# Optimization experiments

Hardware: AMD Instinct MI355X
Metric: run time of the kernel (lower is better)

Reference implementation:

```python
import jax, jax.numpy as jnp
import numpy as np

N_NODES = 20000
N_EDGES = 320000
N_GRAPHS = 64
OBS = 64
EDGE_DIM = 16
HEADS = 4
HID = 64
NEG_SLOPE = 0.2
EPS = 1e-16


def _gat_layer(x, src, dst, edge_attr, W, We, att_src, att_dst, att_edge, b):
    """PyG GATConv (concat=True, eval mode: no dropout).
    x: [N, Fin], edge_attr: [E, De], W: [Fin, H*C], We: [De, H*C],
    att_*: [H, C], b: [H*C]. Returns [N, H*C]."""
    N = x.shape[0]
    h = (x @ W).reshape(N, HEADS, HID)                      # [N,H,C]
    he = (edge_attr @ We).reshape(-1, HEADS, HID)           # [E,H,C]
    a_src = jnp.einsum('nhc,hc->nh', h, att_src)            # [N,H]
    a_dst = jnp.einsum('nhc,hc->nh', h, att_dst)
    a_e = jnp.einsum('ehc,hc->eh', he, att_edge)            # [E,H]
    alpha = a_src[src] + a_dst[dst] + a_e                   # [E,H]
    alpha = jax.nn.leaky_relu(alpha, NEG_SLOPE)
    # segment softmax over destination neighborhoods
    m = jax.ops.segment_max(alpha, dst, num_segments=N)     # [N,H]
    m = jnp.where(jnp.isfinite(m), m, 0.0)
    ea = jnp.exp(alpha - m[dst])
    denom = jax.ops.segment_sum(ea, dst, num_segments=N)    # [N,H]
    alpha = ea / (denom[dst] + EPS)
    msg = h[src] * alpha[:, :, None]                        # [E,H,C]
    out = jax.ops.segment_sum(msg, dst, num_segments=N)     # [N,H,C]
    return out.reshape(N, HEADS * HID) + b


def _make_params(key):
    ks = jax.random.split(key, 18)
    p = {}
    dims_in = [OBS, HEADS * HID, HEADS * HID]
    for i in range(3):
        j = i * 6
        fin = dims_in[i]
        p[f'W{i+1}'] = jax.random.normal(ks[j], (fin, HEADS * HID), jnp.float32) * (1.0 / np.sqrt(fin))
        p[f'We{i+1}'] = jax.random.normal(ks[j+1], (EDGE_DIM, HEADS * HID), jnp.float32) * (1.0 / np.sqrt(EDGE_DIM))
        p[f'att_src{i+1}'] = jax.random.normal(ks[j+2], (HEADS, HID), jnp.float32) * 0.1
        p[f'att_dst{i+1}'] = jax.random.normal(ks[j+3], (HEADS, HID), jnp.float32) * 0.1
        p[f'att_edge{i+1}'] = jax.random.normal(ks[j+4], (HEADS, HID), jnp.float32) * 0.1
        p[f'b{i+1}'] = jnp.zeros((HEADS * HID,), jnp.float32)
    return p


def setup_inputs() -> dict:
    key = jax.random.key(0)
    k1, k2, k3, k4, kp = jax.random.split(key, 5)
    inp = {
        'x': jax.random.normal(k1, (N_NODES, OBS), jnp.float32),
        'edge_index': jax.random.randint(k2, (2, N_EDGES), 0, N_NODES, jnp.int64),
        'edge_attr': jax.random.normal(k3, (N_EDGES, EDGE_DIM), jnp.float32),
        'batch': jnp.sort(jax.random.randint(k4, (N_NODES,), 0, N_GRAPHS, jnp.int64)),
    }
    inp.update(_make_params(kp))
    return inp


def reference(x, edge_index, edge_attr, batch,
              W1, We1, att_src1, att_dst1, att_edge1, b1,
              W2, We2, att_src2, att_dst2, att_edge2, b2,
              W3, We3, att_src3, att_dst3, att_edge3, b3):
    src, dst = edge_index[0], edge_index[1]
    h = jax.nn.relu(_gat_layer(x, src, dst, edge_attr, W1, We1, att_src1, att_dst1, att_edge1, b1))
    h = jax.nn.relu(_gat_layer(h, src, dst, edge_attr, W2, We2, att_src2, att_dst2, att_edge2, b2))
    h = jax.nn.relu(_gat_layer(h, src, dst, edge_attr, W3, We3, att_src3, att_dst3, att_edge3, b3))
    # global mean pool over graphs
    sums = jax.ops.segment_sum(h, batch, num_segments=N_GRAPHS)      # [G, H*C]
    counts = jax.ops.segment_sum(jnp.ones((h.shape[0], 1), h.dtype), batch, num_segments=N_GRAPHS)
    pooled = sums / jnp.maximum(counts, 1.0)
    return jnp.tanh(pooled)
```

## Files before the change

### kernel.cpp

```cpp
#include <hip/hip_runtime.h>
#include <hip/hip_bf16.h>
#include <hip/hip_fp16.h>
#include <math.h>

#define N_NODES 20000
#define N_EDGES 320000
#define N_GRAPHS 64
#define OBS 64
#define EDGE_DIM 16
#define HEADS 4
#define HID 64
#define HC 256
#define NEG_SLOPE 0.2f
#define EPSF 1e-16f
#define N_SCAN_BLOCKS ((N_NODES + 255) / 256)
#define CVT_BLOCKS (N_NODES * OBS / 4 / 256)
#define CAP 64

typedef _Float16 f16x8 __attribute__((ext_vector_type(8)));
typedef float f32x4 __attribute__((ext_vector_type(4)));

__global__ __launch_bounds__(256) void zero3_kernel(int* __restrict__ counts,
                                                    float* __restrict__ pooled,
                                                    int* __restrict__ gcounts) {
    int i = blockIdx.x * 256 + threadIdx.x;
    if (i < N_NODES) counts[i] = 0;
    if (i < N_GRAPHS * HC) pooled[i] = 0.f;
    if (i < N_GRAPHS) gcounts[i] = 0;
}

__global__ __launch_bounds__(256) void cvtwt_kernel(const float* __restrict__ x, __half* __restrict__ x16,
                                                    const float* __restrict__ W0, const float* __restrict__ W1,
                                                    const float* __restrict__ W2,
                                                    __half* __restrict__ wt0, __half* __restrict__ wt1,
                                                    __half* __restrict__ wt2) {
    int b = blockIdx.x, t = threadIdx.x;
    if (b < CVT_BLOCKS) {
        int i = (b * 256 + t) * 4;
        float4 v = *(const float4*)(x + i);
        *(__half2*)(x16 + i)     = __floats2half2_rn(v.x, v.y);
        *(__half2*)(x16 + i + 2) = __floats2half2_rn(v.z, v.w);
    } else if (b < CVT_BLOCKS + OBS) {
        int k = b - CVT_BLOCKS;
        wt0[(size_t)t * OBS + k] = __float2half(W0[(size_t)k * HC + t]);
    } else if (b < CVT_BLOCKS + OBS + HC) {
        int k = b - CVT_BLOCKS - OBS;
        wt1[(size_t)t * HC + k] = __float2half(W1[(size_t)k * HC + t]);
    } else {
        int k = b - CVT_BLOCKS - OBS - HC;
        wt2[(size_t)t * HC + k] = __float2half(W2[(size_t)k * HC + t]);
    }
}

__global__ __launch_bounds__(256) void count_kernel(const int* __restrict__ ei, int* __restrict__ counts) {
    int e = blockIdx.x * 256 + threadIdx.x;
    if (e >= N_EDGES) return;
    atomicAdd(&counts[ei[N_EDGES + e]], 1);
}

__global__ __launch_bounds__(256) void scan_local_kernel(const int* __restrict__ counts,
                                                         int* __restrict__ row_start,
                                                         int* __restrict__ blk_tot) {
    int b = blockIdx.x, t = threadIdx.x;
    int i = b * 256 + t;
    int v = (i < N_NODES) ? counts[i] : 0;
    int lane = t & 63, w = t >> 6;
    int x = v;
    #pragma unroll
    for (int off = 1; off < 64; off <<= 1) {
        int y = __shfl_up(x, off, 64);
        if (lane >= off) x += y;
    }
    __shared__ int wsum[4];
    __shared__ int woff[4];
    if (lane == 63) wsum[w] = x;
    __syncthreads();
    if (t == 0) {
        int s = 0;
        #pragma unroll
        for (int k = 0; k < 4; ++k) { woff[k] = s; s += wsum[k]; }
        blk_tot[b] = s;
    }
    __syncthreads();
    if (i < N_NODES) row_start[i] = x - v + woff[w];
}

__global__ __launch_bounds__(256) void scan_add_kernel(int* __restrict__ row_start,
                                                       const int* __restrict__ blk_tot,
                                                       int* __restrict__ cursor) {
    __shared__ int sd[128];
    int b = blockIdx.x, t = threadIdx.x;
    if (t < 128) sd[t] = (t < b && t < N_SCAN_BLOCKS) ? blk_tot[t] : 0;
    __syncthreads();
    #pragma unroll
    for (int off = 64; off >= 1; off >>= 1) {
        if (t < off) sd[t] += sd[t + off];
        __syncthreads();
    }
    int base = sd[0];
    int i = b * 256 + t;
    if (i < N_NODES) {
        int r = row_start[i] + base;
        row_start[i] = r;
        cursor[i] = r;
    }
}

__global__ __launch_bounds__(256) void fill_kernel(const int* __restrict__ ei,
                                                   int* __restrict__ cursor,
                                                   int* __restrict__ src_csr,
                                                   int* __restrict__ edge_pos) {
    int e = blockIdx.x * 256 + threadIdx.x;
    if (e >= N_EDGES) return;
    int s = ei[e];
    int d = ei[N_EDGES + e];
    int pos = atomicAdd(&cursor[d], 1);
    src_csr[pos] = s;
    edge_pos[e] = pos;
}

__global__ void weff3_kernel(const float* __restrict__ We0, const float* __restrict__ ae0,
                             const float* __restrict__ We1, const float* __restrict__ ae1,
                             const float* __restrict__ We2, const float* __restrict__ ae2,
                             float* __restrict__ w_eff3) {
    int l = blockIdx.x, t = threadIdx.x;
    const float* We = (l == 0) ? We0 : (l == 1) ? We1 : We2;
    const float* ae = (l == 0) ? ae0 : (l == 1) ? ae1 : ae2;
    int hh = t >> 4, d = t & 15;
    float acc = 0.f;
    #pragma unroll 8
    for (int c = 0; c < HID; ++c)
        acc += We[d * HC + hh * HID + c] * ae[hh * HID + c];
    w_eff3[l * 64 + hh * 16 + d] = acc;
}

__global__ __launch_bounds__(256) void ae3_kernel(const float* __restrict__ edge_attr,
                                                  const int* __restrict__ edge_pos,
                                                  const float* __restrict__ w_eff3,
                                                  float4* __restrict__ ae_csr) {
    __shared__ float wsh[192];
    int t = threadIdx.x;
    if (t < 192) wsh[t] = w_eff3[t];
    __syncthreads();
    int e = blockIdx.x * 256 + t;
    if (e >= N_EDGES) return;
    const float* ea = edge_attr + (size_t)e * EDGE_DIM;
    float x[16];
    #pragma unroll
    for (int i = 0; i < 16; i += 4) {
        float4 v = *(const float4*)(ea + i);
        x[i] = v.x; x[i + 1] = v.y; x[i + 2] = v.z; x[i + 3] = v.w;
    }
    int pos = edge_pos[e];
    #pragma unroll
    for (int l = 0; l < 3; ++l) {
        float al[4];
        #pragma unroll
        for (int hh = 0; hh < 4; ++hh) {
            float acc = 0.f;
            #pragma unroll
            for (int i = 0; i < 16; ++i) acc += x[i] * wsh[l * 64 + hh * 16 + i];
            al[hh] = acc;
        }
        ae_csr[(size_t)l * N_EDGES + pos] = make_float4(al[0], al[1], al[2], al[3]);
    }
}

template <int NKT>
__global__ __launch_bounds__(256) void gemm16_kernel(const __half* __restrict__ A16,
                                                     const __half* __restrict__ Wt16,
                                                     __half* __restrict__ C16, int M,
                                                     const float* __restrict__ att_src,
                                                     const float* __restrict__ att_dst,
                                                     float* __restrict__ a_src,
                                                     float* __restrict__ a_dst) {
    constexpr int K = NKT * 32;
    __shared__ __align__(16) _Float16 lds[64 * 264];
    int t = threadIdx.x;
    int w = t >> 6, l = t & 63;
    int cg = l & 15, gg = l >> 4;
    int m0 = blockIdx.x * 64;

    {
        int row = (t >> 6) * 16 + (t & 15);
        int k8 = (t >> 4) & 3;
        int rg = m0 + row;
        if (rg >= M) rg = M - 1;
        const _Float16* ag = (const _Float16*)A16 + (size_t)rg * K + k8 * 8;
        f16x8 tmp[NKT];
        #pragma unroll
        for (int j = 0; j < NKT; ++j) tmp[j] = *(const f16x8*)(ag + j * 32);
        #pragma unroll
        for (int j = 0; j < NKT; ++j) *(f16x8*)&lds[(size_t)(j * 256 + t) * 8] = tmp[j];
    }
    __syncthreads();

    f32x4 acc[4][4] = {};
    const _Float16* bg = (const _Float16*)Wt16 + (size_t)(w * 64 + cg) * K + gg * 8;
    #pragma unroll 2
    for (int kt = 0; kt < NKT; ++kt) {
        f16x8 bf[4], af[4];
        #pragma unroll
        for (int ni = 0; ni < 4; ++ni)
            bf[ni] = *(const f16x8*)(bg + (size_t)(ni * 16) * K + kt * 32);
        #pragma unroll
        for (int mi = 0; mi < 4; ++mi)
            af[mi] = *(const f16x8*)&lds[(size_t)(kt * 256 + mi * 64 + l) * 8];
        #pragma unroll
        for (int mi = 0; mi < 4; ++mi)
            #pragma unroll
            for (int ni = 0; ni < 4; ++ni)
                acc[mi][ni] = __builtin_amdgcn_mfma_f32_16x16x32_f16(af[mi], bf[ni], acc[mi][ni], 0, 0, 0);
    }

    {
        float avs[4], avd[4];
        #pragma unroll
        for (int ni = 0; ni < 4; ++ni) {
            avs[ni] = att_src[w * 64 + ni * 16 + cg];
            avd[ni] = att_dst[w * 64 + ni * 16 + cg];
        }
        #pragma unroll
        for (int mi = 0; mi < 4; ++mi)
            #pragma unroll
            for (int reg = 0; reg < 4; ++reg) {
                float ps = acc[mi][0][reg] * avs[0] + acc[mi][1][reg] * avs[1]
                         + acc[mi][2][reg] * avs[2] + acc[mi][3][reg] * avs[3];
                float pd = acc[mi][0][reg] * avd[0] + acc[mi][1][reg] * avd[1]
                         + acc[mi][2][reg] * avd[2] + acc[mi][3][reg] * avd[3];
                #pragma unroll
                for (int o = 1; o < 16; o <<= 1) {
                    ps += __shfl_xor(ps, o, 64);
                    pd += __shfl_xor(pd, o, 64);
                }
                int m = m0 + mi * 16 + gg * 4 + reg;
                if (cg == 0 && m < M) {
                    a_src[(size_t)m * 4 + w] = ps;
                    a_dst[(size_t)m * 4 + w] = pd;
                }
            }
    }

    __syncthreads();
    #pragma unroll
    for (int mi = 0; mi < 4; ++mi)
        #pragma unroll
        for (int ni = 0; ni < 4; ++ni)
            #pragma unroll
            for (int reg = 0; reg < 4; ++reg) {
                int row = mi * 16 + gg * 4 + reg;
                int col = w * 64 + ni * 16 + cg;
                lds[row * 264 + col] = (_Float16)acc[mi][ni][reg];
            }
    __syncthreads();
    #pragma unroll
    for (int i = 0; i < 8; ++i) {
        int g = i * 256 + t;
        int row = g >> 5, cw = g & 31;
        int m = m0 + row;
        if (m < M) {
            f16x8 v = *(const f16x8*)&lds[row * 264 + cw * 8];
            *(f16x8*)((_Float16*)C16 + (size_t)m * HC + cw * 8) = v;
        }
    }
}

__global__ __launch_bounds__(256) void aggregate3_kernel(const int* __restrict__ src_csr,
                                                         const float4* __restrict__ ae_csr,
                                                         const int* __restrict__ row_start,
                                                         const int* __restrict__ counts,
                                                         const float* __restrict__ a_src,
                                                         const float* __restrict__ a_dst,
                                                         const __half* __restrict__ h16,
                                                         const float* __restrict__ bias,
                                                         __half* __restrict__ out16) {
    __shared__ float wlds[4][4][CAP + 1];
    int wid = threadIdx.x >> 6, lane = threadIdx.x & 63;
    int n = blockIdx.x * 4 + wid;
    int start = row_start[n];
    int deg = counts[n];
    const float4* ae = ae_csr + start;
    const int* sp = src_csr + start;
    float4 ad = *(const float4*)(a_dst + (size_t)n * 4);

    float m0 = -INFINITY, m1 = -INFINITY, m2 = -INFINITY, m3 = -INFINITY;
    for (int i = lane; i < deg; i += 64) {
        float4 a = ae[i];
        int s = sp[i];
        float4 as = *(const float4*)(a_src + (size_t)s * 4);
        float v0 = a.x + as.x + ad.x; v0 = v0 > 0.f ? v0 : NEG_SLOPE * v0;
        float v1 = a.y + as.y + ad.y; v1 = v1 > 0.f ? v1 : NEG_SLOPE * v1;
        float v2 = a.z + as.z + ad.z; v2 = v2 > 0.f ? v2 : NEG_SLOPE * v2;
        float v3 = a.w + as.w + ad.w; v3 = v3 > 0.f ? v3 : NEG_SLOPE * v3;
        if (i < CAP) {
            wlds[wid][0][i] = v0; wlds[wid][1][i] = v1;
            wlds[wid][2][i] = v2; wlds[wid][3][i] = v3;
        }
        m0 = fmaxf(m0, v0); m1 = fmaxf(m1, v1);
        m2 = fmaxf(m2, v2); m3 = fmaxf(m3, v3);
    }
    #pragma unroll
    for (int o = 32; o > 0; o >>= 1) {
        m0 = fmaxf(m0, __shfl_xor(m0, o, 64));
        m1 = fmaxf(m1, __shfl_xor(m1, o, 64));
        m2 = fmaxf(m2, __shfl_xor(m2, o, 64));
        m3 = fmaxf(m3, __shfl_xor(m3, o, 64));
    }

    float d0 = 0.f, d1 = 0.f, d2 = 0.f, d3 = 0.f;
    for (int i = lane; i < deg; i += 64) {
        float v0, v1, v2, v3;
        if (i < CAP) {
            v0 = wlds[wid][0][i]; v1 = wlds[wid][1][i];
            v2 = wlds[wid][2][i]; v3 = wlds[wid][3][i];
        } else {
            float4 a = ae[i];
            int s = sp[i];
            float4 as = *(const float4*)(a_src + (size_t)s * 4);
            v0 = a.x + as.x + ad.x; v0 = v0 > 0.f ? v0 : NEG_SLOPE * v0;
            v1 = a.y + as.y + ad.y; v1 = v1 > 0.f ? v1 : NEG_SLOPE * v1;
            v2 = a.z + as.z + ad.z; v2 = v2 > 0.f ? v2 : NEG_SLOPE * v2;
            v3 = a.w + as.w + ad.w; v3 = v3 > 0.f ? v3 : NEG_SLOPE * v3;
        }
        float e0 = __expf(v0 - m0);
        float e1 = __expf(v1 - m1);
        float e2 = __expf(v2 - m2);
        float e3 = __expf(v3 - m3);
        d0 += e0; d1 += e1; d2 += e2; d3 += e3;
        if (i < CAP) {
            wlds[wid][0][i] = e0; wlds[wid][1][i] = e1;
            wlds[wid][2][i] = e2; wlds[wid][3][i] = e3;
        }
    }
    #pragma unroll
    for (int o = 32; o > 0; o >>= 1) {
        d0 += __shfl_xor(d0, o, 64);
        d1 += __shfl_xor(d1, o, 64);
        d2 += __shfl_xor(d2, o, 64);
        d3 += __shfl_xor(d3, o, 64);
    }

    int g = lane >> 5, j = lane & 31;
    int head = j >> 3;
    float mh = (head < 2) ? (head == 0 ? m0 : m1) : (head == 2 ? m2 : m3);
    float dh = (head < 2) ? (head == 0 ? d0 : d1) : (head == 2 ? d2 : d3);
    float adh = (head < 2) ? (head == 0 ? ad.x : ad.y) : (head == 2 ? ad.z : ad.w);

    float acc[8] = {};
    int niter = (deg + 1) >> 1;
    #pragma unroll 2
    for (int it = 0; it < niter; ++it) {
        int e = it * 2 + g;
        bool valid = e < deg;
        int ec = valid ? e : deg - 1;
        int s = sp[ec];
        float wgt;
        if (ec < CAP) {
            wgt = wlds[wid][head][ec];
        } else {
            float4 a = ae[ec];
            float aa = (head < 2) ? (head == 0 ? a.x : a.y) : (head == 2 ? a.z : a.w);
            const float* asp = a_src + (size_t)s * 4;
            float v = aa + asp[head] + adh;
            v = v > 0.f ? v : NEG_SLOPE * v;
            wgt = __expf(v - mh);
        }
        if (!valid) wgt = 0.f;
        f16x8 hv = *(const f16x8*)((const _Float16*)h16 + (size_t)s * HC + j * 8);
        #pragma unroll
        for (int q = 0; q < 8; ++q) acc[q] += wgt * (float)hv[q];
    }
    #pragma unroll
    for (int q = 0; q < 8; ++q) acc[q] += __shfl_xor(acc[q], 32, 64);

    if (g == 0) {
        float invd = 1.f / (dh + EPSF);
        float4 b0 = *(const float4*)(bias + j * 8);
        float4 b1 = *(const float4*)(bias + j * 8 + 4);
        float r[8];
        r[0] = fmaxf(acc[0] * invd + b0.x, 0.f);
        r[1] = fmaxf(acc[1] * invd + b0.y, 0.f);
        r[2] = fmaxf(acc[2] * invd + b0.z, 0.f);
        r[3] = fmaxf(acc[3] * invd + b0.w, 0.f);
        r[4] = fmaxf(acc[4] * invd + b1.x, 0.f);
        r[5] = fmaxf(acc[5] * invd + b1.y, 0.f);
        r[6] = fmaxf(acc[6] * invd + b1.z, 0.f);
        r[7] = fmaxf(acc[7] * invd + b1.w, 0.f);
        f16x8 o;
        #pragma unroll
        for (int q = 0; q < 8; ++q) o[q] = (_Float16)r[q];
        *(f16x8*)((_Float16*)out16 + (size_t)n * HC + j * 8) = o;
    }
}

#define NPB 100
__global__ __launch_bounds__(256) void pool_kernel(const __half* __restrict__ h,
                                                   const int* __restrict__ batch,
                                                   float* __restrict__ pooled,
                                                   int* __restrict__ gcounts) {
    int t = threadIdx.x;
    int n0 = blockIdx.x * NPB;
    int n1 = n0 + NPB;
    if (n1 > N_NODES) n1 = N_NODES;
    if (n0 >= N_NODES) return;
    int cur = batch[n0];
    float acc = 0.f;
    int cnt = 0;
    for (int n = n0; n < n1; ++n) {
        int g = batch[n];
        if (g != cur) {
            atomicAdd(&pooled[cur * HC + t], acc);
            if (t == 0) atomicAdd(&gcounts[cur], cnt);
            acc = 0.f; cnt = 0; cur = g;
        }
        acc += __half2float(h[(size_t)n * HC + t]);
        cnt++;
    }
    atomicAdd(&pooled[cur * HC + t], acc);
    if (t == 0) atomicAdd(&gcounts[cur], cnt);
}

__global__ __launch_bounds__(256) void finalize_kernel(const float* __restrict__ pooled,
                                                       const int* __restrict__ gcounts,
                                                       float* __restrict__ out) {
    int g = blockIdx.x, t = threadIdx.x;
    float c = (float)(gcounts[g] > 1 ? gcounts[g] : 1);
    out[g * HC + t] = tanhf(pooled[g * HC + t] / c);
}

extern "C" void kernel_launch(void* const* d_in, const int* in_sizes, int n_in,
                              void* d_out, int out_size, void* d_ws, size_t ws_size,
                              hipStream_t stream) {
    const float* x         = (const float*)d_in[0];
    const int*   ei        = (const int*)d_in[1];
    const float* edge_attr = (const float*)d_in[2];
    const int*   batch     = (const int*)d_in[3];
    const float* Wl[3]  = {(const float*)d_in[4],  (const float*)d_in[10], (const float*)d_in[16]};
    const float* Wel[3] = {(const float*)d_in[5],  (const float*)d_in[11], (const float*)d_in[17]};
    const float* asl[3] = {(const float*)d_in[6],  (const float*)d_in[12], (const float*)d_in[18]};
    const float* adl[3] = {(const float*)d_in[7],  (const float*)d_in[13], (const float*)d_in[19]};
    const float* ael[3] = {(const float*)d_in[8],  (const float*)d_in[14], (const float*)d_in[20]};
    const float* bl[3]  = {(const float*)d_in[9],  (const float*)d_in[15], (const float*)d_in[21]};
    float* out = (float*)d_out;

    char* p = (char*)d_ws;
    auto alloc = [&](size_t bytes) -> void* {
        void* r = (void*)p;
        p += (bytes + 255) & ~(size_t)255;
        return r;
    };
    __half* x16       = (__half*)alloc((size_t)N_NODES * OBS * 2);
    __half* hA16      = (__half*)alloc((size_t)N_NODES * HC * 2);
    __half* hB16      = (__half*)alloc((size_t)N_NODES * HC * 2);
    __half* wt0       = (__half*)alloc((size_t)HC * OBS * 2);
    __half* wt1       = (__half*)alloc((size_t)HC * HC * 2);
    __half* wt2       = (__half*)alloc((size_t)HC * HC * 2);
    float* a_src      = (float*)alloc((size_t)N_NODES * 4 * 4);
    float* a_dst      = (float*)alloc((size_t)N_NODES * 4 * 4);
    float4* ae_csr    = (float4*)alloc((size_t)3 * N_EDGES * 16);
    int* counts       = (int*)alloc((size_t)N_NODES * 4);
    int* row_start    = (int*)alloc((size_t)N_NODES * 4);
    int* cursor       = (int*)alloc((size_t)N_NODES * 4);
    int* src_csr      = (int*)alloc((size_t)N_EDGES * 4);
    int* edge_pos     = (int*)alloc((size_t)N_EDGES * 4);
    float* w_eff3     = (float*)alloc(192 * 4);
    float* pooled     = (float*)alloc((size_t)N_GRAPHS * HC * 4);
    int* gcounts      = (int*)alloc((size_t)N_GRAPHS * 4);
    int* blk_tot      = (int*)alloc((size_t)N_SCAN_BLOCKS * 4);

    zero3_kernel<<<N_SCAN_BLOCKS, 256, 0, stream>>>(counts, pooled, gcounts);
    cvtwt_kernel<<<CVT_BLOCKS + OBS + HC + HC, 256, 0, stream>>>(x, x16, Wl[0], Wl[1], Wl[2],
                                                                 wt0, wt1, wt2);
    weff3_kernel<<<3, 64, 0, stream>>>(Wel[0], ael[0], Wel[1], ael[1], Wel[2], ael[2], w_eff3);

    count_kernel<<<N_EDGES / 256, 256, 0, stream>>>(ei, counts);
    scan_local_kernel<<<N_SCAN_BLOCKS, 256, 0, stream>>>(counts, row_start, blk_tot);
    scan_add_kernel<<<N_SCAN_BLOCKS, 256, 0, stream>>>(row_start, blk_tot, cursor);
    fill_kernel<<<N_EDGES / 256, 256, 0, stream>>>(ei, cursor, src_csr, edge_pos);

    ae3_kernel<<<N_EDGES / 256, 256, 0, stream>>>(edge_attr, edge_pos, w_eff3, ae_csr);

    const int ngrid = (N_NODES + 63) / 64;
    const __half* wtl[3] = {wt0, wt1, wt2};
    const __half* cur_in = x16;
    for (int l = 0; l < 3; ++l) {
        if (l == 0)
            gemm16_kernel<2><<<ngrid, 256, 0, stream>>>(cur_in, wtl[l], hA16, N_NODES,
                                                        asl[l], adl[l], a_src, a_dst);
        else
            gemm16_kernel<8><<<ngrid, 256, 0, stream>>>(cur_in, wtl[l], hA16, N_NODES,
                                                        asl[l], adl[l], a_src, a_dst);
        aggregate3_kernel<<<N_NODES / 4, 256, 0, stream>>>(src_csr, ae_csr + (size_t)l * N_EDGES,
                                                           row_start, counts, a_src, a_dst,
                                                           hA16, bl[l], hB16);
        cur_in = hB16;
    }

    pool_kernel<<<(N_NODES + NPB - 1) / NPB, 256, 0, stream>>>(hB16, batch, pooled, gcounts);
    finalize_kernel<<<N_GRAPHS, 256, 0, stream>>>(pooled, gcounts, out);
}
```

Before: 244.5 us.

## Fuse setup kernels, merge CSR fill with edge-attention, batch aggregation gathers

```diff
diff --git a/kernel.cpp b/kernel.cpp
--- a/kernel.cpp
+++ b/kernel.cpp
@@ -20,35 +20,55 @@
 typedef _Float16 f16x8 __attribute__((ext_vector_type(8)));
 typedef float f32x4 __attribute__((ext_vector_type(4)));
 
-__global__ __launch_bounds__(256) void zero3_kernel(int* __restrict__ counts,
+#define SB_ZERO  N_SCAN_BLOCKS
+#define SB_CVT   (SB_ZERO + CVT_BLOCKS)
+#define SB_WT0   (SB_CVT + OBS)
+#define SB_WT1   (SB_WT0 + HC)
+#define SB_WT2   (SB_WT1 + HC)
+#define SB_TOT   (SB_WT2 + 3)
+__global__ __launch_bounds__(256) void setup_kernel(int* __restrict__ counts,
                                                     float* __restrict__ pooled,
-                                                    int* __restrict__ gcounts) {
-    int i = blockIdx.x * 256 + threadIdx.x;
-    if (i < N_NODES) counts[i] = 0;
-    if (i < N_GRAPHS * HC) pooled[i] = 0.f;
-    if (i < N_GRAPHS) gcounts[i] = 0;
-}
-
-__global__ __launch_bounds__(256) void cvtwt_kernel(const float* __restrict__ x, __half* __restrict__ x16,
+                                                    int* __restrict__ gcounts,
+                                                    const float* __restrict__ x, __half* __restrict__ x16,
                                                     const float* __restrict__ W0, const float* __restrict__ W1,
                                                     const float* __restrict__ W2,
                                                     __half* __restrict__ wt0, __half* __restrict__ wt1,
-                                                    __half* __restrict__ wt2) {
+                                                    __half* __restrict__ wt2,
+                                                    const float* __restrict__ We0, const float* __restrict__ ae0,
+                                                    const float* __restrict__ We1, const float* __restrict__ ae1,
+                                                    const float* __restrict__ We2, const float* __restrict__ ae2,
+                                                    float* __restrict__ w_eff3) {
     int b = blockIdx.x, t = threadIdx.x;
-    if (b < CVT_BLOCKS) {
-        int i = (b * 256 + t) * 4;
+    if (b < SB_ZERO) {
+        int i = b * 256 + t;
+        if (i < N_NODES) counts[i] = 0;
+        if (i < N_GRAPHS * HC) pooled[i] = 0.f;
+        if (i < N_GRAPHS) gcounts[i] = 0;
+    } else if (b < SB_CVT) {
+        int i = ((b - SB_ZERO) * 256 + t) * 4;
         float4 v = *(const float4*)(x + i);
         *(__half2*)(x16 + i)     = __floats2half2_rn(v.x, v.y);
         *(__half2*)(x16 + i + 2) = __floats2half2_rn(v.z, v.w);
-    } else if (b < CVT_BLOCKS + OBS) {
-        int k = b - CVT_BLOCKS;
+    } else if (b < SB_WT0) {
+        int k = b - SB_CVT;
         wt0[(size_t)t * OBS + k] = __float2half(W0[(size_t)k * HC + t]);
-    } else if (b < CVT_BLOCKS + OBS + HC) {
-        int k = b - CVT_BLOCKS - OBS;
+    } else if (b < SB_WT1) {
+        int k = b - SB_WT0;
         wt1[(size_t)t * HC + k] = __float2half(W1[(size_t)k * HC + t]);
+    } else if (b < SB_WT2) {
+        int k = b - SB_WT1;
+        wt2[(size_t)t * HC + k] = __float2half(W2[(size_t)k * HC + t]);
     } else {
-        int k = b - CVT_BLOCKS - OBS - HC;
-        wt2[(size_t)t * HC + k] = __float2half(W2[(size_t)k * HC + t]);
+        int l = b - SB_WT2;
+        if (t >= 64) return;
+        const float* We = (l == 0) ? We0 : (l == 1) ? We1 : We2;
+        const float* ae = (l == 0) ? ae0 : (l == 1) ? ae1 : ae2;
+        int hh = t >> 4, d = t & 15;
+        float acc = 0.f;
+        #pragma unroll 8
+        for (int c = 0; c < HID; ++c)
+            acc += We[d * HC + hh * HID + c] * ae[hh * HID + c];
+        w_eff3[l * 64 + hh * 16 + d] = acc;
     }
 }
 
@@ -106,44 +126,22 @@
     }
 }
 
-__global__ __launch_bounds__(256) void fill_kernel(const int* __restrict__ ei,
-                                                   int* __restrict__ cursor,
-                                                   int* __restrict__ src_csr,
-                                                   int* __restrict__ edge_pos) {
-    int e = blockIdx.x * 256 + threadIdx.x;
+__global__ __launch_bounds__(256) void fill_ae_kernel(const int* __restrict__ ei,
+                                                      const float* __restrict__ edge_attr,
+                                                      const float* __restrict__ w_eff3,
+                                                      int* __restrict__ cursor,
+                                                      int* __restrict__ src_csr,
+                                                      float4* __restrict__ ae_csr) {
+    __shared__ float wsh[192];
+    int t = threadIdx.x;
+    if (t < 192) wsh[t] = w_eff3[t];
+    __syncthreads();
+    int e = blockIdx.x * 256 + t;
     if (e >= N_EDGES) return;
     int s = ei[e];
     int d = ei[N_EDGES + e];
     int pos = atomicAdd(&cursor[d], 1);
     src_csr[pos] = s;
-    edge_pos[e] = pos;
-}
-
-__global__ void weff3_kernel(const float* __restrict__ We0, const float* __restrict__ ae0,
-                             const float* __restrict__ We1, const float* __restrict__ ae1,
-                             const float* __restrict__ We2, const float* __restrict__ ae2,
-                             float* __restrict__ w_eff3) {
-    int l = blockIdx.x, t = threadIdx.x;
-    const float* We = (l == 0) ? We0 : (l == 1) ? We1 : We2;
-    const float* ae = (l == 0) ? ae0 : (l == 1) ? ae1 : ae2;
-    int hh = t >> 4, d = t & 15;
-    float acc = 0.f;
-    #pragma unroll 8
-    for (int c = 0; c < HID; ++c)
-        acc += We[d * HC + hh * HID + c] * ae[hh * HID + c];
-    w_eff3[l * 64 + hh * 16 + d] = acc;
-}
-
-__global__ __launch_bounds__(256) void ae3_kernel(const float* __restrict__ edge_attr,
-                                                  const int* __restrict__ edge_pos,
-                                                  const float* __restrict__ w_eff3,
-                                                  float4* __restrict__ ae_csr) {
-    __shared__ float wsh[192];
-    int t = threadIdx.x;
-    if (t < 192) wsh[t] = w_eff3[t];
-    __syncthreads();
-    int e = blockIdx.x * 256 + t;
-    if (e >= N_EDGES) return;
     const float* ea = edge_attr + (size_t)e * EDGE_DIM;
     float x[16];
     #pragma unroll
@@ -151,7 +149,6 @@
         float4 v = *(const float4*)(ea + i);
         x[i] = v.x; x[i + 1] = v.y; x[i + 2] = v.z; x[i + 3] = v.w;
     }
-    int pos = edge_pos[e];
     #pragma unroll
     for (int l = 0; l < 3; ++l) {
         float al[4];
@@ -265,7 +262,7 @@
     }
 }
 
-__global__ __launch_bounds__(256) void aggregate3_kernel(const int* __restrict__ src_csr,
+__global__ __launch_bounds__(256) void aggregate4_kernel(const int* __restrict__ src_csr,
                                                          const float4* __restrict__ ae_csr,
                                                          const int* __restrict__ row_start,
                                                          const int* __restrict__ counts,
@@ -348,27 +345,60 @@
 
     float acc[8] = {};
     int niter = (deg + 1) >> 1;
-    #pragma unroll 2
-    for (int it = 0; it < niter; ++it) {
-        int e = it * 2 + g;
-        bool valid = e < deg;
-        int ec = valid ? e : deg - 1;
-        int s = sp[ec];
-        float wgt;
-        if (ec < CAP) {
-            wgt = wlds[wid][head][ec];
-        } else {
-            float4 a = ae[ec];
-            float aa = (head < 2) ? (head == 0 ? a.x : a.y) : (head == 2 ? a.z : a.w);
-            const float* asp = a_src + (size_t)s * 4;
-            float v = aa + asp[head] + adh;
-            v = v > 0.f ? v : NEG_SLOPE * v;
-            wgt = __expf(v - mh);
-        }
-        if (!valid) wgt = 0.f;
-        f16x8 hv = *(const f16x8*)((const _Float16*)h16 + (size_t)s * HC + j * 8);
-        #pragma unroll
-        for (int q = 0; q < 8; ++q) acc[q] += wgt * (float)hv[q];
+    if (deg <= CAP) {
+        int it = 0;
+        for (; it + 4 <= niter; it += 4) {
+            int s_[4]; float w_[4]; f16x8 hv_[4];
+            #pragma unroll
+            for (int u = 0; u < 4; ++u) {
+                int e = (it + u) * 2 + g;
+                bool valid = e < deg;
+                int ec = valid ? e : deg - 1;
+                s_[u] = sp[ec];
+                float wv = wlds[wid][head][ec];
+                w_[u] = valid ? wv : 0.f;
+            }
+            #pragma unroll
+            for (int u = 0; u < 4; ++u)
+                hv_[u] = *(const f16x8*)((const _Float16*)h16 + (size_t)s_[u] * HC + j * 8);
+            #pragma unroll
+            for (int u = 0; u < 4; ++u)
+                #pragma unroll
+                for (int q = 0; q < 8; ++q) acc[q] += w_[u] * (float)hv_[u][q];
+        }
+        for (; it < niter; ++it) {
+            int e = it * 2 + g;
+            bool valid = e < deg;
+            int ec = valid ? e : deg - 1;
+            int s = sp[ec];
+            float wv = wlds[wid][head][ec];
+            float wgt = valid ? wv : 0.f;
+            f16x8 hv = *(const f16x8*)((const _Float16*)h16 + (size_t)s * HC + j * 8);
+            #pragma unroll
+            for (int q = 0; q < 8; ++q) acc[q] += wgt * (float)hv[q];
+        }
+    } else {
+        for (int it = 0; it < niter; ++it) {
+            int e = it * 2 + g;
+            bool valid = e < deg;
+            int ec = valid ? e : deg - 1;
+            int s = sp[ec];
+            float wgt;
+            if (ec < CAP) {
+                wgt = wlds[wid][head][ec];
+            } else {
+                float4 a = ae[ec];
+                float aa = (head < 2) ? (head == 0 ? a.x : a.y) : (head == 2 ? a.z : a.w);
+                const float* asp = a_src + (size_t)s * 4;
+                float v = aa + asp[head] + adh;
+                v = v > 0.f ? v : NEG_SLOPE * v;
+                wgt = __expf(v - mh);
+            }
+            if (!valid) wgt = 0.f;
+            f16x8 hv = *(const f16x8*)((const _Float16*)h16 + (size_t)s * HC + j * 8);
+            #pragma unroll
+            for (int q = 0; q < 8; ++q) acc[q] += wgt * (float)hv[q];
+        }
     }
     #pragma unroll
     for (int q = 0; q < 8; ++q) acc[q] += __shfl_xor(acc[q], 32, 64);
@@ -462,23 +492,21 @@
     int* row_start    = (int*)alloc((size_t)N_NODES * 4);
     int* cursor       = (int*)alloc((size_t)N_NODES * 4);
     int* src_csr      = (int*)alloc((size_t)N_EDGES * 4);
-    int* edge_pos     = (int*)alloc((size_t)N_EDGES * 4);
     float* w_eff3     = (float*)alloc(192 * 4);
     float* pooled     = (float*)alloc((size_t)N_GRAPHS * HC * 4);
     int* gcounts      = (int*)alloc((size_t)N_GRAPHS * 4);
     int* blk_tot      = (int*)alloc((size_t)N_SCAN_BLOCKS * 4);
 
-    zero3_kernel<<<N_SCAN_BLOCKS, 256, 0, stream>>>(counts, pooled, gcounts);
-    cvtwt_kernel<<<CVT_BLOCKS + OBS + HC + HC, 256, 0, stream>>>(x, x16, Wl[0], Wl[1], Wl[2],
-                                                                 wt0, wt1, wt2);
-    weff3_kernel<<<3, 64, 0, stream>>>(Wel[0], ael[0], Wel[1], ael[1], Wel[2], ael[2], w_eff3);
+    setup_kernel<<<SB_TOT, 256, 0, stream>>>(counts, pooled, gcounts, x, x16,
+                                             Wl[0], Wl[1], Wl[2], wt0, wt1, wt2,
+                                             Wel[0], ael[0], Wel[1], ael[1], Wel[2], ael[2],
+                                             w_eff3);
 
     count_kernel<<<N_EDGES / 256, 256, 0, stream>>>(ei, counts);
     scan_local_kernel<<<N_SCAN_BLOCKS, 256, 0, stream>>>(counts, row_start, blk_tot);
     scan_add_kernel<<<N_SCAN_BLOCKS, 256, 0, stream>>>(row_start, blk_tot, cursor);
-    fill_kernel<<<N_EDGES / 256, 256, 0, stream>>>(ei, cursor, src_csr, edge_pos);
-
-    ae3_kernel<<<N_EDGES / 256, 256, 0, stream>>>(edge_attr, edge_pos, w_eff3, ae_csr);
+    fill_ae_kernel<<<N_EDGES / 256, 256, 0, stream>>>(ei, edge_attr, w_eff3, cursor,
+                                                      src_csr, ae_csr);
 
     const int ngrid = (N_NODES + 63) / 64;
     const __half* wtl[3] = {wt0, wt1, wt2};
@@ -490,7 +518,7 @@
         else
             gemm16_kernel<8><<<ngrid, 256, 0, stream>>>(cur_in, wtl[l], hA16, N_NODES,
                                                         asl[l], adl[l], a_src, a_dst);
-        aggregate3_kernel<<<N_NODES / 4, 256, 0, stream>>>(src_csr, ae_csr + (size_t)l * N_EDGES,
+        aggregate4_kernel<<<N_NODES / 4, 256, 0, stream>>>(src_csr, ae_csr + (size_t)l * N_EDGES,
                                                            row_start, counts, a_src, a_dst,
                                                            hA16, bl[l], hB16);
         cur_in = hB16;
```

Result: faster. 226.5 us (-7.4%).
